# Kernel tuning notes

Measured on AMD Instinct MI355X. Metric: run time of the kernel, lower is better.

The kernel has to match this reference:

```python
import jax, jax.numpy as jnp
import numpy as np

B, T, H, D_IN, D_OUT = 128, 2048, 512, 40, 1


def setup_inputs() -> dict:
    key = jax.random.key(0)
    ks = jax.random.split(key, 11)
    x = jax.random.normal(ks[0], (B, T, D_IN), dtype=jnp.float32)
    s_in = 1.0 / np.sqrt(D_IN // 2)
    s_h = 1.0 / np.sqrt(H)
    W1 = jax.random.uniform(ks[1], (H, D_IN // 2), minval=-s_in, maxval=s_in, dtype=jnp.float32)
    b1 = jax.random.uniform(ks[2], (H,), minval=-s_in, maxval=s_in, dtype=jnp.float32)
    W2 = jax.random.uniform(ks[3], (H, D_IN // 2), minval=-s_in, maxval=s_in, dtype=jnp.float32)
    b2 = jax.random.uniform(ks[4], (H,), minval=-s_in, maxval=s_in, dtype=jnp.float32)
    Wo = jax.random.uniform(ks[5], (D_OUT, H), minval=-s_h, maxval=s_h, dtype=jnp.float32)
    bo = jax.random.uniform(ks[6], (D_OUT,), minval=-s_h, maxval=s_h, dtype=jnp.float32)
    tau_m = jax.random.uniform(ks[7], (H,), minval=0.0, maxval=4.0, dtype=jnp.float32)
    tau_n1 = jax.random.uniform(ks[8], (H,), minval=2.0, maxval=6.0, dtype=jnp.float32)  # beneficial_init: slow branch
    tau_n2 = jax.random.uniform(ks[9], (H,), minval=-4.0, maxval=0.0, dtype=jnp.float32)  # fast branch
    return {"x": x, "W1": W1, "b1": b1, "W2": W2, "b2": b2,
            "Wo": Wo, "bo": bo, "tau_m": tau_m, "tau_n1": tau_n1, "tau_n2": tau_n2}


def reference(x, W1, b1, W2, b2, Wo, bo, tau_m, tau_n1, tau_n2):
    # Precompute per-timestep dense projections as single big GEMMs (same math as per-step Linear).
    d1_in = jnp.einsum('btd,hd->bth', x[..., :20], W1) + b1  # [B,T,H]
    d2_in = jnp.einsum('btd,hd->bth', x[..., 20:], W2) + b2  # [B,T,H]
    beta1 = jax.nn.sigmoid(tau_n1)
    beta2 = jax.nn.sigmoid(tau_n2)
    alpha = jax.nn.sigmoid(tau_m)
    bsz = x.shape[0]
    z = jnp.zeros((bsz, tau_m.shape[0]), dtype=x.dtype)

    def step(carry, inp):
        d1, d2, mem = carry
        i1, i2 = inp
        d1 = beta1 * d1 + (1.0 - beta1) * i1
        d2 = beta2 * d2 + (1.0 - beta2) * i2
        mem = alpha * mem + (1.0 - alpha) * (d1 + d2)
        return (d1, d2, mem), mem

    # time-major scan over seq_len
    _, mems = jax.lax.scan(step, (z, z, z),
                           (jnp.swapaxes(d1_in, 0, 1), jnp.swapaxes(d2_in, 0, 1)))  # mems: [T,B,H]
    out = jax.nn.sigmoid(jnp.einsum('tbh,oh->tbo', mems, Wo) + bo)  # [T,B,1]
    return jnp.swapaxes(out, 0, 1)  # [B,T,1]
```

## Files before the change

kernel.cpp:

```cpp
#include <hip/hip_runtime.h>
#include <math.h>


#define B_   128
#define T_   2048
#define DIN  40
#define L_   192
#define XROWS 704
#define GROWS 228
#define GOFFD 14080
#define LDSDW (GOFFD + GROWS * 20)

typedef __attribute__((ext_vector_type(8))) short short8;
typedef __attribute__((ext_vector_type(4))) float f32x4;

__device__ __align__(16) float d_g[L_ * DIN];
__device__ float d_c[T_];

__device__ __forceinline__ float sigmf(float v) { return 1.f / (1.f + __expf(-v)); }
__device__ __forceinline__ int div5(int v) { return (v * 3277) >> 14; }

__device__ __forceinline__ unsigned pk2bf(float lo, float hi) {
#if defined(__has_builtin) && __has_builtin(__builtin_amdgcn_cvt_pk_bf16_f32)
    typedef __bf16 bf2_t __attribute__((ext_vector_type(2)));
    bf2_t r = __builtin_amdgcn_cvt_pk_bf16_f32(lo, hi);
    return __builtin_bit_cast(unsigned, r);
#else
    unsigned a = __float_as_uint(lo) + 0x8000u;
    unsigned b = __float_as_uint(hi) + 0x8000u;
    return __builtin_amdgcn_perm(b, a, 0x07060302);
#endif
}

__global__ __launch_bounds__(256) void prepG(
    const float* __restrict__ W1, const float* __restrict__ b1v,
    const float* __restrict__ W2, const float* __restrict__ b2v,
    const float* __restrict__ Wo, const float* __restrict__ bo,
    const float* __restrict__ tau_m, const float* __restrict__ tau_n1,
    const float* __restrict__ tau_n2)
{
    const int blk = blockIdx.x, tid = threadIdx.x;
    if (blk < 40) {
        __shared__ float cw[512], laG[512], lbG[512];
        const int d = blk;
        const int dm = (d < 20) ? d : d - 20;
        for (int i = 0; i < 2; ++i) {
            const int h = tid + 256 * i;
            const float a = sigmf(tau_m[h]);
            float bb = sigmf((d < 20) ? tau_n1[h] : tau_n2[h]);
            float diff = a - bb;
            if (fabsf(diff) < 1e-5f) { bb = a - 1e-5f; diff = 1e-5f; }
            const float w = (d < 20) ? W1[h * 20 + dm] : W2[h * 20 + dm];
            cw[h]  = Wo[h] * (1.f - a) * (1.f - bb) * w / diff;
            laG[h] = log2f(a);
            lbG[h] = log2f(bb);
        }
        __syncthreads();
        if (tid < 192) {
            const float fs1 = (float)(tid + 1);
            float acc = 0.f;
            for (int h = 0; h < 512; ++h)
                acc += cw[h] * (exp2f(fs1 * laG[h]) - exp2f(fs1 * lbG[h]));
            d_g[tid * 40 + d] = acc;
        }
    } else {
        __shared__ float As[512], B1s[512], B2s[512], cst[512],
                         laC[512], lb1C[512], lb2C[512];
        __shared__ float red[8][32];
        for (int i = 0; i < 2; ++i) {
            const int h = tid + 256 * i;
            const float a = sigmf(tau_m[h]);
            float b1c = sigmf(tau_n1[h]); float d1 = a - b1c;
            if (fabsf(d1) < 1e-5f) { b1c = a - 1e-5f; d1 = 1e-5f; }
            float b2c = sigmf(tau_n2[h]); float d2 = a - b2c;
            if (fabsf(d2) < 1e-5f) { b2c = a - 1e-5f; d2 = 1e-5f; }
            const float wv = Wo[h], bb1 = b1v[h], bb2 = b2v[h];
            As[h]  = wv * (bb1 * a * (1.f - b1c) / d1 + bb2 * a * (1.f - b2c) / d2);
            B1s[h] = wv * bb1 * b1c * (1.f - a) / d1;
            B2s[h] = wv * bb2 * b2c * (1.f - a) / d2;
            cst[h] = wv * (bb1 + bb2);
            laC[h] = log2f(a); lb1C[h] = log2f(b1c); lb2C[h] = log2f(b2c);
        }
        __syncthreads();
        const int tl = tid & 31;
        const int hc = tid >> 5;
        const float ft1 = (float)((blk - 40) * 32 + tl + 1);
        float acc = 0.f;
        for (int hh = 0; hh < 64; ++hh) {
            const int h = hc * 64 + hh;
            acc += cst[h] - As[h] * exp2f(ft1 * laC[h])
                 + B1s[h] * exp2f(ft1 * lb1C[h])
                 + B2s[h] * exp2f(ft1 * lb2C[h]);
        }
        red[hc][tl] = acc;
        __syncthreads();
        if (tid < 32) {
            float s = bo[0];
#pragma unroll
            for (int c = 0; c < 8; ++c) s += red[c][tid];
            d_c[(blk - 40) * 32 + tid] = s;
        }
    }
}

__global__ __launch_bounds__(512, 2) void fir_mfma(const float* __restrict__ x,
                                                   float* __restrict__ out)
{
    __shared__ __align__(16) unsigned int lds[LDSDW];

    const int blk = blockIdx.x;
    const int b   = blk >> 2;
    const int t0  = (blk & 3) << 9;
    const int tid = threadIdx.x;
    const int lid = tid & 63;
    const int wv  = tid >> 6;
    const int rl  = lid & 15;
    const int g4  = (lid >> 4) & 3;

    const float4* __restrict__ xf4 = (const float4*)(x + (size_t)b * (T_ * DIN));
    const float4* __restrict__ gf4 = (const float4*)d_g;

#pragma unroll
    for (int it = 0; it < 7; ++it) {
        const int i = tid + 512 * it;
        if (i < XROWS * 5) {
            const int w  = div5(i);
            const int dq = i - 5 * w;
            const int t  = t0 - 191 + w;
            float4 v0 = make_float4(0.f, 0.f, 0.f, 0.f), v1 = v0;
            if (t >= 0 && t < T_) { v0 = xf4[t * 10 + dq * 2]; v1 = xf4[t * 10 + dq * 2 + 1]; }
            const int rid = (w & 15) * 44 + (w >> 4);
            const int tsl = dq + rid;
            const int sl  = tsl - 5 * div5(tsl);
            uint4 pv = { pk2bf(v0.x, v0.y), pk2bf(v0.z, v0.w),
                         pk2bf(v1.x, v1.y), pk2bf(v1.z, v1.w) };
            *(uint4*)&lds[rid * 20 + sl * 4] = pv;
        }
    }
#pragma unroll
    for (int it = 0; it < 3; ++it) {
        const int i = tid + 512 * it;
        if (i < GROWS * 5) {
            const int gr = div5(i);
            const int dq = i - 5 * gr;
            const int s  = gr - 16;
            float4 v0 = make_float4(0.f, 0.f, 0.f, 0.f), v1 = v0;
            if (s >= 0 && s < L_) { v0 = gf4[s * 10 + dq * 2]; v1 = gf4[s * 10 + dq * 2 + 1]; }
            const int tsl = dq + gr;
            const int sl  = tsl - 5 * div5(tsl);
            uint4 pv = { pk2bf(v0.x, v0.y), pk2bf(v0.z, v0.w),
                         pk2bf(v1.x, v1.y), pk2bf(v1.z, v1.w) };
            *(uint4*)&lds[GOFFD + gr * 20 + sl * 4] = pv;
        }
    }
    __syncthreads();

    f32x4 acc0 = { 0.f, 0.f, 0.f, 0.f };
    f32x4 acc1 = { 0.f, 0.f, 0.f, 0.f };
    const int kc0 = 33 * wv;
#pragma unroll 3
    for (int s = 0; s < 33; ++s) {
        const int p  = 4 * (kc0 + s) + g4;
        const int sq = div5(p);
        const int db = p - 5 * sq;
        const int gr  = sq + rl;
        const int tb  = db + gr;
        const int slb = tb - 5 * div5(tb);
        const short8 gb = *(const short8*)&lds[GOFFD + gr * 20 + slb * 4];
        const int m   = 207 - sq;
        const int rid = (m & 15) * 44 + (m >> 4) + rl;
        const int ta  = db + rid;
        const int sa0 = ta - 5 * div5(ta);
        const short8 xa0 = *(const short8*)&lds[rid * 20 + sa0 * 4];
        int sa1 = sa0 + 1; sa1 = (sa1 == 5) ? 0 : sa1;
        const short8 xa1 = *(const short8*)&lds[(rid + 16) * 20 + sa1 * 4];
        acc0 = __builtin_amdgcn_mfma_f32_16x16x32_bf16(xa0, gb, acc0, 0, 0, 0);
        acc1 = __builtin_amdgcn_mfma_f32_16x16x32_bf16(xa1, gb, acc1, 0, 0, 0);
    }

    __syncthreads();
    {
        float* lf = (float*)lds;
#pragma unroll
        for (int q = 0; q < 4; ++q) {
            lf[((0 * 64 + lid) * 4 + q) * 9 + wv] = acc0[q];
            lf[((1 * 64 + lid) * 4 + q) * 9 + wv] = acc1[q];
        }
    }
    __syncthreads();
    {
        const int o   = tid;
        const int tau = o >> 8, oin = o & 255;
        const int r   = oin >> 4, cc = oin & 15;
        const int lane = ((r >> 2) << 4) | cc;
        const int reg  = r & 3;
        const int Lx   = (tau * 64 + lane) * 4 + reg;
        const float* lf = (const float*)lds;
        float sacc = 0.f;
#pragma unroll
        for (int w2 = 0; w2 < 8; ++w2) sacc += lf[Lx * 9 + w2];
        out[(size_t)b * T_ + t0 + o] = sigmf(sacc + d_c[t0 + o]);
    }
}

extern "C" void kernel_launch(void* const* d_in, const int* in_sizes, int n_in,
                              void* d_out, int out_size, void* d_ws, size_t ws_size,
                              hipStream_t stream)
{
    const float* x      = (const float*)d_in[0];
    const float* W1     = (const float*)d_in[1];
    const float* b1     = (const float*)d_in[2];
    const float* W2     = (const float*)d_in[3];
    const float* b2     = (const float*)d_in[4];
    const float* Wo     = (const float*)d_in[5];
    const float* bo     = (const float*)d_in[6];
    const float* tau_m  = (const float*)d_in[7];
    const float* tau_n1 = (const float*)d_in[8];
    const float* tau_n2 = (const float*)d_in[9];

    hipLaunchKernelGGL(prepG, dim3(104), dim3(256), 0, stream,
                       W1, b1, W2, b2, Wo, bo, tau_m, tau_n1, tau_n2);
    hipLaunchKernelGGL(fir_mfma, dim3(512), dim3(512), 0, stream,
                       x, (float*)d_out);
}
```

Before: 126.1 us.

## Fuse coefficient prep and FIR MFMA into one kernel with atomic-flag sync

Merges the prep kernel into the main FIR kernel. The first 104 blocks compute the FIR taps and the time-dependent constants. Every block then stages its x tile into LDS and spins on a global completion counter before loading the taps. A per-launch ticket counter keeps repeated launches apart. This removes the second kernel launch and the gap between launches, and lets x loading overlap with the prep work. The cost is a spin-wait that relies on the prep blocks being co-resident or scheduled first, plus extra atomics.

```diff
diff --git a/kernel.cpp b/kernel.cpp
--- a/kernel.cpp
+++ b/kernel.cpp
@@ -16,6 +16,8 @@
 
 __device__ __align__(16) float d_g[L_ * DIN];
 __device__ float d_c[T_];
+__device__ unsigned d_ticket = 0;
+__device__ unsigned d_done   = 0;
 
 __device__ __forceinline__ float sigmf(float v) { return 1.f / (1.f + __expf(-v)); }
 __device__ __forceinline__ int div5(int v) { return (v * 3277) >> 14; }
@@ -32,20 +34,31 @@
 #endif
 }
 
-__global__ __launch_bounds__(256) void prepG(
+__global__ __launch_bounds__(512, 2) void sfnn_one(
+    const float* __restrict__ x,
     const float* __restrict__ W1, const float* __restrict__ b1v,
     const float* __restrict__ W2, const float* __restrict__ b2v,
     const float* __restrict__ Wo, const float* __restrict__ bo,
     const float* __restrict__ tau_m, const float* __restrict__ tau_n1,
-    const float* __restrict__ tau_n2)
+    const float* __restrict__ tau_n2,
+    float* __restrict__ out)
 {
-    const int blk = blockIdx.x, tid = threadIdx.x;
+    __shared__ __align__(16) unsigned int lds[LDSDW];
+
+    const int blk = blockIdx.x;
+    const int tid = threadIdx.x;
+
+    unsigned runv = 0;
+    if (tid == 0) runv = atomicAdd(&d_ticket, 1u) >> 9;
+
     if (blk < 40) {
-        __shared__ float cw[512], laG[512], lbG[512];
+        float* cw  = (float*)lds;
+        float* laG = cw + 512;
+        float* lbG = cw + 1024;
         const int d = blk;
         const int dm = (d < 20) ? d : d - 20;
-        for (int i = 0; i < 2; ++i) {
-            const int h = tid + 256 * i;
+        {
+            const int h = tid;
             const float a = sigmf(tau_m[h]);
             float bb = sigmf((d < 20) ? tau_n1[h] : tau_n2[h]);
             float diff = a - bb;
@@ -63,12 +76,20 @@
                 acc += cw[h] * (exp2f(fs1 * laG[h]) - exp2f(fs1 * lbG[h]));
             d_g[tid * 40 + d] = acc;
         }
-    } else {
-        __shared__ float As[512], B1s[512], B2s[512], cst[512],
-                         laC[512], lb1C[512], lb2C[512];
-        __shared__ float red[8][32];
-        for (int i = 0; i < 2; ++i) {
-            const int h = tid + 256 * i;
+        __threadfence();
+        __syncthreads();
+        if (tid == 0) atomicAdd(&d_done, 1u);
+    } else if (blk < 104) {
+        float* As   = (float*)lds;
+        float* B1s  = As + 512;
+        float* B2s  = As + 1024;
+        float* cst  = As + 1536;
+        float* laC  = As + 2048;
+        float* lb1C = As + 2560;
+        float* lb2C = As + 3072;
+        float* red  = As + 3584;
+        {
+            const int h = tid;
             const float a = sigmf(tau_m[h]);
             float b1c = sigmf(tau_n1[h]); float d1 = a - b1c;
             if (fabsf(d1) < 1e-5f) { b1c = a - 1e-5f; d1 = 1e-5f; }
@@ -86,32 +107,27 @@
         const int hc = tid >> 5;
         const float ft1 = (float)((blk - 40) * 32 + tl + 1);
         float acc = 0.f;
-        for (int hh = 0; hh < 64; ++hh) {
-            const int h = hc * 64 + hh;
+        for (int hh = 0; hh < 32; ++hh) {
+            const int h = hc * 32 + hh;
             acc += cst[h] - As[h] * exp2f(ft1 * laC[h])
                  + B1s[h] * exp2f(ft1 * lb1C[h])
                  + B2s[h] * exp2f(ft1 * lb2C[h]);
         }
-        red[hc][tl] = acc;
+        red[hc * 32 + tl] = acc;
         __syncthreads();
         if (tid < 32) {
             float s = bo[0];
 #pragma unroll
-            for (int c = 0; c < 8; ++c) s += red[c][tid];
+            for (int c = 0; c < 16; ++c) s += red[c * 32 + tid];
             d_c[(blk - 40) * 32 + tid] = s;
         }
-    }
-}
-
-__global__ __launch_bounds__(512, 2) void fir_mfma(const float* __restrict__ x,
-                                                   float* __restrict__ out)
-{
-    __shared__ __align__(16) unsigned int lds[LDSDW];
-
-    const int blk = blockIdx.x;
+        __threadfence();
+        __syncthreads();
+        if (tid == 0) atomicAdd(&d_done, 1u);
+    }
+
     const int b   = blk >> 2;
     const int t0  = (blk & 3) << 9;
-    const int tid = threadIdx.x;
     const int lid = tid & 63;
     const int wv  = tid >> 6;
     const int rl  = lid & 15;
@@ -137,6 +153,16 @@
             *(uint4*)&lds[rid * 20 + sl * 4] = pv;
         }
     }
+
+    if (tid == 0) {
+        const unsigned target = 104u * (runv + 1u);
+        while (__hip_atomic_load(&d_done, __ATOMIC_ACQUIRE,
+                                 __HIP_MEMORY_SCOPE_AGENT) < target)
+            __builtin_amdgcn_s_sleep(2);
+        __threadfence();
+    }
+    __syncthreads();
+
 #pragma unroll
     for (int it = 0; it < 3; ++it) {
         const int i = tid + 512 * it;
@@ -218,8 +244,7 @@
     const float* tau_n1 = (const float*)d_in[8];
     const float* tau_n2 = (const float*)d_in[9];
 
-    hipLaunchKernelGGL(prepG, dim3(104), dim3(256), 0, stream,
-                       W1, b1, W2, b2, Wo, bo, tau_m, tau_n1, tau_n2);
-    hipLaunchKernelGGL(fir_mfma, dim3(512), dim3(512), 0, stream,
-                       x, (float*)d_out);
+    hipLaunchKernelGGL(sfnn_one, dim3(512), dim3(512), 0, stream,
+                       x, W1, b1, W2, b2, Wo, bo, tau_m, tau_n1, tau_n2,
+                       (float*)d_out);
 }
```

Measured after the change: 170.4 us. +35.1%, slower.
